# Optimization experiments

Measured on AMD Instinct MI355X. Metric: run time of the kernel, lower is better.

## Reference

```python
import jax, jax.numpy as jnp
import numpy as np


def rotate_half(x):
    d = x.shape[-1] // 2
    return jnp.concatenate([-x[..., d:], x[..., :d]], axis=-1)


def setup_inputs() -> dict:
    key = jax.random.key(0)
    ks = jax.random.split(key, 8)
    B, T, C, H = 2, 2048, 2048, 16
    hd = C // H
    x = jax.random.normal(ks[0], (B, T, C), dtype=jnp.float32)
    # realistic RoPE tables
    inv_freq = 1.0 / (10000.0 ** (jnp.arange(0, hd, 2, dtype=jnp.float32) / hd))
    t = jnp.arange(T, dtype=jnp.float32)
    freqs = jnp.einsum('t,f->tf', t, inv_freq)
    emb = jnp.concatenate([freqs, freqs], axis=-1)  # [T, hd]
    cos = jnp.cos(emb)
    sin = jnp.sin(emb)
    mask = jnp.tril(jnp.ones((T, T), dtype=bool))[None, None]  # causal [1,1,T,T]
    s = C ** -0.5
    Wq = jax.random.normal(ks[1], (C, C), dtype=jnp.float32) * s
    Wk = jax.random.normal(ks[2], (C, C), dtype=jnp.float32) * s
    Wv = jax.random.normal(ks[3], (C, C), dtype=jnp.float32) * s
    Wo = jax.random.normal(ks[4], (C, C), dtype=jnp.float32) * s
    return {"x": x, "cos": cos, "sin": sin, "mask": mask,
            "Wq": Wq, "Wk": Wk, "Wv": Wv, "Wo": Wo}


def reference(x, cos, sin, mask, Wq, Wk, Wv, Wo):
    B, T, C = x.shape
    H = 16
    hd = C // H
    scale = hd ** -0.5
    # projections: torch Linear stores W as [out,in], y = x @ W^T
    def proj(W):
        return jnp.einsum('btc,dc->btd', x, W).reshape(B, T, H, hd).transpose(0, 2, 1, 3)
    q, k, v = proj(Wq), proj(Wk), proj(Wv)  # [B,H,T,hd]
    c = cos[None, None]  # [1,1,T,hd]
    s = sin[None, None]
    q = q * c + rotate_half(q) * s
    k = k * c + rotate_half(k) * s
    attn = jnp.einsum('bhqd,bhkd->bhqk', q, k) * scale
    attn = jnp.where(mask, attn, -jnp.inf)
    attn = jax.nn.softmax(attn, axis=-1)
    out = jnp.einsum('bhqk,bhkd->bhqd', attn, v)
    out = out.transpose(0, 2, 1, 3).reshape(B, T, C)
    return jnp.einsum('btc,dc->btd', out, Wo)
```

## Files before the change

### kernel.cpp

```cpp
#include <hip/hip_runtime.h>
#include <cstdint>

typedef __bf16 bf16_t;
typedef __bf16 bf16x8 __attribute__((ext_vector_type(8)));
typedef __bf16 bf16x4 __attribute__((ext_vector_type(4)));
typedef float  f32x4  __attribute__((ext_vector_type(4)));

#define BB 2
#define TT 2048
#define CC 2048
#define HH 16
#define HD 128

static __device__ __forceinline__ void async_copy16(const void* gp, void* lp) {
  __builtin_amdgcn_global_load_lds(
      (const __attribute__((address_space(1))) void*)(uintptr_t)gp,
      (__attribute__((address_space(3))) void*)(uint32_t)(uintptr_t)lp,
      16, 0, 0);
}

__global__ __launch_bounds__(256)
void cast_all(const float* __restrict__ x, const float* __restrict__ wq,
              const float* __restrict__ wk, const float* __restrict__ wv,
              const float* __restrict__ wo, bf16_t* __restrict__ xb,
              bf16_t* __restrict__ wq_b) {
  const int NX4 = (BB * TT * CC) / 4;
  const int NW4 = (CC * CC) / 4;
  int i = blockIdx.x * 256 + threadIdx.x;
  const float* s;
  bf16_t* d;
  int off;
  if (i < NX4) {
    s = x; d = xb; off = i;
  } else {
    int j = i - NX4;
    int w = j >> 20;
    off = j & (NW4 - 1);
    s = (w == 0) ? wq : (w == 1) ? wk : (w == 2) ? wv : wo;
    d = wq_b + (size_t)w * (CC * CC);
  }
  float4 v = ((const float4*)s)[off];
  bf16x4 o;
  o[0] = (bf16_t)v.x; o[1] = (bf16_t)v.y; o[2] = (bf16_t)v.z; o[3] = (bf16_t)v.w;
  ((bf16x4*)d)[off] = o;
}

template <int MODE>
__global__ __launch_bounds__(256)
void gemm_bt(const bf16_t* __restrict__ A, const bf16_t* __restrict__ Bw,
             void* __restrict__ C0, void* __restrict__ C1, void* __restrict__ C2,
             int Kdim, int Ndim) {
  __shared__ __align__(16) char smem[128 * 136 * 2];
  bf16_t* As = (bf16_t*)smem;
  bf16_t* Bs = (bf16_t*)(smem + 16384);
  const int tid  = threadIdx.x;
  const int wave = tid >> 6, lane = tid & 63;
  const int quad = lane >> 4, l16 = lane & 15;
  const int m0 = blockIdx.y * 128, n0 = blockIdx.x * 128;
  const int wm = (wave >> 1) * 64, wn = (wave & 1) * 64;

  f32x4 acc[4][4] = {};

  const int srow = lane >> 3;
  const int scol = (((lane & 7) ^ srow) & 7) * 8;
  const int swz  = (l16 & 7) * 8;

  for (int k0 = 0; k0 < Kdim; k0 += 64) {
#pragma unroll
    for (int i = 0; i < 4; ++i) {
      int chunk = wave * 4 + i;
      int row = chunk * 8 + srow;
      async_copy16(A + (size_t)(m0 + row) * Kdim + k0 + scol, As + chunk * 512);
    }
#pragma unroll
    for (int i = 0; i < 4; ++i) {
      int chunk = wave * 4 + i;
      int row = chunk * 8 + srow;
      async_copy16(Bw + (size_t)(n0 + row) * Kdim + k0 + scol, Bs + chunk * 512);
    }
    __syncthreads();
#pragma unroll
    for (int kk = 0; kk < 64; kk += 32) {
      const int koff = (kk + quad * 8) ^ swz;
      bf16x8 af[4], bfr[4];
#pragma unroll
      for (int i = 0; i < 4; ++i)
        af[i] = *(const bf16x8*)&As[(wm + i * 16 + l16) * 64 + koff];
#pragma unroll
      for (int j = 0; j < 4; ++j)
        bfr[j] = *(const bf16x8*)&Bs[(wn + j * 16 + l16) * 64 + koff];
#pragma unroll
      for (int i = 0; i < 4; ++i)
#pragma unroll
        for (int j = 0; j < 4; ++j)
          acc[i][j] = __builtin_amdgcn_mfma_f32_16x16x32_bf16(af[i], bfr[j], acc[i][j], 0, 0, 0);
    }
    __syncthreads();
  }

#pragma unroll
  for (int i = 0; i < 4; ++i)
#pragma unroll
    for (int j = 0; j < 4; ++j) {
      int gcol = n0 + wn + j * 16 + l16;
#pragma unroll
      for (int r = 0; r < 4; ++r) {
        int grow = m0 + wm + i * 16 + quad * 4 + r;
        ((float*)C0)[(size_t)grow * Ndim + gcol] = acc[i][j][r];
      }
    }
}

__global__ __launch_bounds__(512, 2)
void gemm_qkv256(const bf16_t* __restrict__ A, const bf16_t* __restrict__ Bw,
                 bf16_t* __restrict__ Qo, bf16_t* __restrict__ Ko,
                 bf16_t* __restrict__ Vo, int Kdim) {
  extern __shared__ __align__(16) char smem[];
  bf16_t* lds = (bf16_t*)smem;
  const int tid  = threadIdx.x;
  const int wave = tid >> 6, lane = tid & 63;
  const int quad = lane >> 4, l16 = lane & 15;
  const int wm = wave >> 2, wn = wave & 3;
  const int n0 = blockIdx.x * 256, m0 = blockIdx.y * 256;

  const int srow = lane >> 3;
  const int scol = ((lane & 7) ^ srow) * 8;
  const int swz  = (l16 & 7) * 8;
  const int nK = Kdim >> 6;

  const bf16_t* Ag = A  + (size_t)(m0 + wave * 32 + srow) * Kdim + scol;
  const bf16_t* Bg = Bw + (size_t)(n0 + wave * 32 + srow) * Kdim + scol;
  const int ldsChunk = wave * 4 * 512;

#define STAGE_A(kt, buf)                                                      \
  {                                                                           \
    bf16_t* dstA = lds + (buf) * 32768 + ldsChunk;                            \
    const bf16_t* srcA = Ag + (kt) * 64;                                      \
    _Pragma("unroll")                                                         \
    for (int ci = 0; ci < 4; ++ci)                                            \
      async_copy16(srcA + (size_t)(ci * 8) * Kdim, dstA + ci * 512);          \
  }
#define STAGE_B(kt, buf)                                                      \
  {                                                                           \
    bf16_t* dstB = lds + (buf) * 32768 + 16384 + ldsChunk;                    \
    const bf16_t* srcB = Bg + (kt) * 64;                                      \
    _Pragma("unroll")                                                         \
    for (int ci = 0; ci < 4; ++ci)                                            \
      async_copy16(srcB + (size_t)(ci * 8) * Kdim, dstB + ci * 512);          \
  }

  f32x4 acc[8][4] = {};

  STAGE_A(0, 0); STAGE_B(0, 0); STAGE_A(1, 1); STAGE_B(1, 1);

  const int k0off = (quad * 8) ^ swz;
  const int k1off = (32 + quad * 8) ^ swz;

  for (int k = 0; k < nK; ++k) {
    const int cur = k & 1;
    const bf16_t* Asb = lds + cur * 32768;
    const bf16_t* Bsb = Asb + 16384;
    if (k < nK - 1) asm volatile("s_waitcnt vmcnt(8)" ::: "memory");
    else            asm volatile("s_waitcnt vmcnt(0)" ::: "memory");
    __builtin_amdgcn_s_barrier();
    __builtin_amdgcn_sched_barrier(0);

    bf16x8 a0[8], b0[4], a1[8], b1[4];
#pragma unroll
    for (int i = 0; i < 8; ++i)
      a0[i] = *(const bf16x8*)&Asb[(wm * 128 + i * 16 + l16) * 64 + k0off];
#pragma unroll
    for (int j = 0; j < 4; ++j)
      b0[j] = *(const bf16x8*)&Bsb[(wn * 64 + j * 16 + l16) * 64 + k0off];
    asm volatile("s_waitcnt lgkmcnt(0)" ::: "memory");
    __builtin_amdgcn_sched_barrier(0);
    __builtin_amdgcn_s_setprio(1);
#pragma unroll
    for (int i = 0; i < 4; ++i)
#pragma unroll
      for (int j = 0; j < 4; ++j)
        acc[i][j] = __builtin_amdgcn_mfma_f32_16x16x32_bf16(a0[i], b0[j], acc[i][j], 0, 0, 0);
    __builtin_amdgcn_s_setprio(0);

#pragma unroll
    for (int i = 0; i < 8; ++i)
      a1[i] = *(const bf16x8*)&Asb[(wm * 128 + i * 16 + l16) * 64 + k1off];
#pragma unroll
    for (int j = 0; j < 4; ++j)
      b1[j] = *(const bf16x8*)&Bsb[(wn * 64 + j * 16 + l16) * 64 + k1off];
    __builtin_amdgcn_s_setprio(1);
#pragma unroll
    for (int i = 4; i < 8; ++i)
#pragma unroll
      for (int j = 0; j < 4; ++j)
        acc[i][j] = __builtin_amdgcn_mfma_f32_16x16x32_bf16(a0[i], b0[j], acc[i][j], 0, 0, 0);
    __builtin_amdgcn_s_setprio(0);
    asm volatile("s_waitcnt lgkmcnt(0)" ::: "memory");
    __builtin_amdgcn_s_barrier();
    __builtin_amdgcn_sched_barrier(0);

    if (k + 2 < nK) STAGE_A(k + 2, cur);
    __builtin_amdgcn_s_setprio(1);
#pragma unroll
    for (int i = 0; i < 4; ++i)
#pragma unroll
      for (int j = 0; j < 4; ++j)
        acc[i][j] = __builtin_amdgcn_mfma_f32_16x16x32_bf16(a1[i], b1[j], acc[i][j], 0, 0, 0);
    __builtin_amdgcn_s_setprio(0);

    if (k + 2 < nK) STAGE_B(k + 2, cur);
    __builtin_amdgcn_s_setprio(1);
#pragma unroll
    for (int i = 4; i < 8; ++i)
#pragma unroll
      for (int j = 0; j < 4; ++j)
        acc[i][j] = __builtin_amdgcn_mfma_f32_16x16x32_bf16(a1[i], b1[j], acc[i][j], 0, 0, 0);
    __builtin_amdgcn_s_setprio(0);
  }
#undef STAGE_A
#undef STAGE_B

  const int proj = n0 >> 11;
  if (proj < 2) {
    bf16_t* dst = proj == 0 ? Qo : Ko;
#pragma unroll
    for (int i = 0; i < 8; ++i)
#pragma unroll
      for (int j = 0; j < 4; ++j) {
        int colv = (n0 & (CC - 1)) + wn * 64 + j * 16 + l16;
        int h = colv >> 7, d = colv & (HD - 1);
#pragma unroll
        for (int r = 0; r < 4; ++r) {
          int grow = m0 + wm * 128 + i * 16 + quad * 4 + r;
          int b = grow >> 11, t = grow & (TT - 1);
          dst[(((size_t)(b * HH + h) * TT + t) * HD) + d] = (bf16_t)acc[i][j][r];
        }
      }
  } else {
    bf16_t* Ct = (bf16_t*)smem;
    const int b = m0 >> 11;
#pragma unroll
    for (int p = 0; p < 2; ++p) {
      __syncthreads();
      if (wm == p) {
#pragma unroll
        for (int i = 0; i < 8; ++i)
#pragma unroll
          for (int j = 0; j < 4; ++j) {
            int c = wn * 64 + j * 16 + l16;
#pragma unroll
            for (int r = 0; r < 4; ++r)
              Ct[(i * 16 + quad * 4 + r) * 264 + c] = (bf16_t)acc[i][j][r];
          }
      }
      __syncthreads();
      const unsigned short* Cu = (const unsigned short*)Ct;
      int c  = tid & 255;
      int rh = (tid >> 8) * 64;
      int dv = (n0 & (CC - 1)) + c;
      int h = dv >> 7, d = dv & (HD - 1);
      unsigned int pk[32];
#pragma unroll
      for (int s = 0; s < 32; ++s) {
        unsigned int lo = Cu[(rh + 2 * s) * 264 + c];
        unsigned int hi = Cu[(rh + 2 * s + 1) * 264 + c];
        pk[s] = lo | (hi << 16);
      }
      bf16_t* dstp = Vo + ((size_t)(b * HH + h) * HD + d) * TT +
                     (m0 & (TT - 1)) + p * 128 + rh;
#pragma unroll
      for (int u = 0; u < 8; ++u) {
        uint4 w; w.x = pk[4*u]; w.y = pk[4*u+1]; w.z = pk[4*u+2]; w.w = pk[4*u+3];
        *(uint4*)(dstp + 8 * u) = w;
      }
    }
  }
}

__global__ __launch_bounds__(256) void rope_kernel(bf16_t* __restrict__ Q, bf16_t* __restrict__ K,
                                                   const float* __restrict__ cosT,
                                                   const float* __restrict__ sinT) {
  int idx = blockIdx.x * 256 + threadIdx.x;
  int d  = idx & 63;
  int t  = (idx >> 6) & (TT - 1);
  int bh = idx >> 17;
  size_t base = ((size_t)bh * TT + t) * HD;
  float c0 = cosT[t * HD + d],      s0 = sinT[t * HD + d];
  float c1 = cosT[t * HD + 64 + d], s1 = sinT[t * HD + 64 + d];
  float q0 = Q[base + d], q1 = Q[base + 64 + d];
  Q[base + d]      = (bf16_t)(q0 * c0 - q1 * s0);
  Q[base + 64 + d] = (bf16_t)(q1 * c1 + q0 * s1);
  float k0 = K[base + d], k1 = K[base + 64 + d];
  K[base + d]      = (bf16_t)(k0 * c0 - k1 * s0);
  K[base + 64 + d] = (bf16_t)(k1 * c1 + k0 * s1);
}

__global__ __launch_bounds__(512, 2)
void attn_kernel(const bf16_t* __restrict__ Q, const bf16_t* __restrict__ K,
                 const bf16_t* __restrict__ Vt, bf16_t* __restrict__ Out) {
  __shared__ __align__(16) bf16_t Ks[2][64 * 128];
  __shared__ __align__(16) bf16_t Vs[2][128 * 64];
  __shared__ __align__(16) bf16_t Pl[8][16 * 72];
  const int lane = threadIdx.x & 63, wave = threadIdx.x >> 6;
  const int quad = lane >> 4, l16 = lane & 15;
  const int linear = blockIdx.x;
  const int hb = linear & 31;
  const int h = hb & (HH - 1), b = hb >> 4;
  const int spair = linear >> 5;
  const size_t qkbase = (size_t)(b * HH + h) * TT * HD;
  const bf16_t* Kh = K + qkbase;
  const bf16_t* Vh = Vt + (size_t)(b * HH + h) * HD * TT;
  const float scale = 0.08838834764831845f;

  const int srK = lane >> 4;
  const int sgK = lane & 15;
  const int scK0 = (sgK ^ srK) * 8;
  const int scK1 = (sgK ^ (4 + srK)) * 8;
  const int srV = lane >> 3;
  const int scV = (((lane & 7) ^ srV) & 7) * 8;
  const int swz = (l16 & 7) * 8;

#pragma unroll
  for (int half = 0; half < 2; ++half) {
    const int qt = half == 0 ? (15 - spair) : spair;
    const int q0 = qt * 128 + wave * 16;
    const int nIter = qt * 2 + 2;

    bf16x8 qf[4];
    {
      const bf16_t* qrow = Q + qkbase + (size_t)(q0 + l16) * HD;
#pragma unroll
      for (int kc = 0; kc < 4; ++kc) qf[kc] = *(const bf16x8*)(qrow + kc * 32 + quad * 8);
    }

    f32x4 o[8] = {};
    float l_i[4] = {};

    {
#pragma unroll
      for (int i = 0; i < 2; ++i) {
        int chunk = wave * 2 + i;
        int sc = (chunk & 1) ? scK1 : scK0;
        async_copy16(Kh + (size_t)(chunk * 4 + srK) * HD + sc, &Ks[0][chunk * 512]);
      }
#pragma unroll
      for (int i = 0; i < 2; ++i) {
        int chunk = wave * 2 + i;
        async_copy16(Vh + (size_t)(chunk * 8 + srV) * TT + scV, &Vs[0][chunk * 512]);
      }
    }

    for (int it = 0; it < nIter; ++it) {
      const int cur = it & 1;
      const int key0 = it * 64;
      __syncthreads();

      if (it + 1 < nIter) {
        const int nxt = cur ^ 1;
        const int knxt = key0 + 64;
#pragma unroll
        for (int i = 0; i < 2; ++i) {
          int chunk = wave * 2 + i;
          int sc = (chunk & 1) ? scK1 : scK0;
          async_copy16(Kh + (size_t)(knxt + chunk * 4 + srK) * HD + sc, &Ks[nxt][chunk * 512]);
        }
#pragma unroll
        for (int i = 0; i < 2; ++i) {
          int chunk = wave * 2 + i;
          async_copy16(Vh + (size_t)(chunk * 8 + srV) * TT + knxt + scV, &Vs[nxt][chunk * 512]);
        }
      }

      f32x4 s[4] = {};
#pragma unroll
      for (int kc = 0; kc < 4; ++kc) {
        const int koff = (kc * 32 + quad * 8) ^ swz;
#pragma unroll
        for (int kt = 0; kt < 4; ++kt) {
          bf16x8 kf = *(const bf16x8*)&Ks[cur][(kt * 16 + l16) * 128 + koff];
          s[kt] = __builtin_amdgcn_mfma_f32_16x16x32_bf16(qf[kc], kf, s[kt], 0, 0, 0);
        }
      }

      {
        bf16_t* pl = &Pl[wave][0];
#pragma unroll
        for (int r = 0; r < 4; ++r) {
          int rel = q0 + quad * 4 + r - key0;
          int prow = (quad * 4 + r) * 72;
          float lr = 0.f;
#pragma unroll
          for (int kt = 0; kt < 4; ++kt) {
            int c16 = kt * 16 + l16;
            float e = (c16 > rel) ? 0.f : __expf(s[kt][r] * scale);
            lr += e;
            pl[prow + c16] = (bf16_t)e;
          }
          l_i[r] += lr;
        }
      }

      bf16x8 pf0 = *(const bf16x8*)&Pl[wave][l16 * 72 + quad * 8];
      bf16x8 pf1 = *(const bf16x8*)&Pl[wave][l16 * 72 + 32 + quad * 8];
      const int voff0 = (quad * 8) ^ swz;
      const int voff1 = (32 + quad * 8) ^ swz;
#pragma unroll
      for (int n = 0; n < 8; ++n) {
        bf16x8 vf0 = *(const bf16x8*)&Vs[cur][(n * 16 + l16) * 64 + voff0];
        bf16x8 vf1 = *(const bf16x8*)&Vs[cur][(n * 16 + l16) * 64 + voff1];
        o[n] = __builtin_amdgcn_mfma_f32_16x16x32_bf16(pf0, vf0, o[n], 0, 0, 0);
        o[n] = __builtin_amdgcn_mfma_f32_16x16x32_bf16(pf1, vf1, o[n], 0, 0, 0);
      }
    }

#pragma unroll
    for (int r = 0; r < 4; ++r) {
      float l = l_i[r];
#pragma unroll
      for (int off = 1; off < 16; off <<= 1) l += __shfl_xor(l, off);
      l_i[r] = 1.f / l;
    }

#pragma unroll
    for (int n = 0; n < 8; ++n)
#pragma unroll
      for (int r = 0; r < 4; ++r) {
        int qg = q0 + quad * 4 + r;
        size_t off = ((size_t)(b * TT + qg) * CC) + h * HD + n * 16 + l16;
        Out[off] = (bf16_t)(o[n][r] * l_i[r]);
      }
  }
}

extern "C" void kernel_launch(void* const* d_in, const int* in_sizes, int n_in,
                              void* d_out, int out_size, void* d_ws, size_t ws_size,
                              hipStream_t stream) {
  const float* x    = (const float*)d_in[0];
  const float* cosT = (const float*)d_in[1];
  const float* sinT = (const float*)d_in[2];
  const float* Wq = (const float*)d_in[4];
  const float* Wk = (const float*)d_in[5];
  const float* Wv = (const float*)d_in[6];
  const float* Wo = (const float*)d_in[7];
  float* out = (float*)d_out;

  char* ws = (char*)d_ws;
  const size_t XSZ = (size_t)BB * TT * CC * 2;
  const size_t WSZ = (size_t)CC * CC * 2;
  bf16_t* x_bf  = (bf16_t*)(ws);
  bf16_t* wq_bf = (bf16_t*)(ws + XSZ);
  bf16_t* wo_bf = (bf16_t*)(ws + XSZ + 3 * WSZ);
  bf16_t* Qb    = (bf16_t*)(ws + XSZ + 4 * WSZ);
  bf16_t* Kb    = (bf16_t*)(ws + 2 * XSZ + 4 * WSZ);
  bf16_t* Vt    = (bf16_t*)(ws + 3 * XSZ + 4 * WSZ);
  bf16_t* attn_bf = x_bf;

  const int NX = BB * TT * CC;
  const int NW = CC * CC;
  cast_all<<<(NX / 4 + 4 * (NW / 4)) / 256, 256, 0, stream>>>(
      x, Wq, Wk, Wv, Wo, x_bf, wq_bf);

  (void)hipFuncSetAttribute(reinterpret_cast<const void*>(gemm_qkv256),
                            hipFuncAttributeMaxDynamicSharedMemorySize, 131072);
  gemm_qkv256<<<dim3(3 * CC / 256, BB * TT / 256), 512, 131072, stream>>>(
      x_bf, wq_bf, Qb, Kb, Vt, CC);

  rope_kernel<<<(BB * HH * TT * 64) / 256, 256, 0, stream>>>(Qb, Kb, cosT, sinT);

  attn_kernel<<<dim3(BB * HH * 8), 512, 0, stream>>>(Qb, Kb, Vt, attn_bf);

  gemm_bt<0><<<dim3(CC / 128, BB * TT / 128), 256, 0, stream>>>(
      attn_bf, wo_bf, out, nullptr, nullptr, CC, CC);
}
```

Before: 375.0 us.

## Split V projection into separate 128-tile GEMM and vectorize RoPE kernel

The fused QKV GEMM now computes only Q and K, giving a 16x16 grid of 256-wide tiles. V is produced by the 128x128 gemm_bt kernel in a new mode that transposes through LDS into the Vt layout. This targets the partial final wave of the 24x16 fused grid, at the cost of an extra launch and a smaller-tile GEMM for V. The RoPE kernel now handles 8 elements per thread with 16-byte loads and stores instead of scalar accesses.

```diff
diff --git a/kernel.cpp b/kernel.cpp
--- a/kernel.cpp
+++ b/kernel.cpp
@@ -98,23 +98,56 @@
     __syncthreads();
   }
 
-#pragma unroll
-  for (int i = 0; i < 4; ++i)
-#pragma unroll
-    for (int j = 0; j < 4; ++j) {
-      int gcol = n0 + wn + j * 16 + l16;
-#pragma unroll
-      for (int r = 0; r < 4; ++r) {
-        int grow = m0 + wm + i * 16 + quad * 4 + r;
-        ((float*)C0)[(size_t)grow * Ndim + gcol] = acc[i][j][r];
-      }
-    }
+  if (MODE == 0) {
+#pragma unroll
+    for (int i = 0; i < 4; ++i)
+#pragma unroll
+      for (int j = 0; j < 4; ++j) {
+        int gcol = n0 + wn + j * 16 + l16;
+#pragma unroll
+        for (int r = 0; r < 4; ++r) {
+          int grow = m0 + wm + i * 16 + quad * 4 + r;
+          ((float*)C0)[(size_t)grow * Ndim + gcol] = acc[i][j][r];
+        }
+      }
+  } else {
+    const int h = (n0 & (CC - 1)) >> 7;
+    bf16_t* Ct = (bf16_t*)smem;
+    __syncthreads();
+#pragma unroll
+    for (int i = 0; i < 4; ++i)
+#pragma unroll
+      for (int j = 0; j < 4; ++j) {
+        int c = wn + j * 16 + l16;
+#pragma unroll
+        for (int r = 0; r < 4; ++r)
+          Ct[(wm + i * 16 + quad * 4 + r) * 136 + c] = (bf16_t)acc[i][j][r];
+      }
+    __syncthreads();
+    const unsigned short* Cu = (const unsigned short*)Ct;
+    int col = tid >> 1;
+    int rh  = (tid & 1) * 64;
+    int grow0 = m0 + rh;
+    int b = grow0 >> 11, t0 = grow0 & (TT - 1);
+    unsigned int pk[32];
+#pragma unroll
+    for (int s = 0; s < 32; ++s) {
+      unsigned int lo = Cu[(rh + 2 * s) * 136 + col];
+      unsigned int hi = Cu[(rh + 2 * s + 1) * 136 + col];
+      pk[s] = lo | (hi << 16);
+    }
+    bf16_t* dstp = (bf16_t*)C2 + ((size_t)(b * HH + h) * HD + col) * TT + t0;
+#pragma unroll
+    for (int u = 0; u < 8; ++u) {
+      uint4 w; w.x = pk[4*u]; w.y = pk[4*u+1]; w.z = pk[4*u+2]; w.w = pk[4*u+3];
+      *(uint4*)(dstp + 8 * u) = w;
+    }
+  }
 }
 
 __global__ __launch_bounds__(512, 2)
 void gemm_qkv256(const bf16_t* __restrict__ A, const bf16_t* __restrict__ Bw,
-                 bf16_t* __restrict__ Qo, bf16_t* __restrict__ Ko,
-                 bf16_t* __restrict__ Vo, int Kdim) {
+                 bf16_t* __restrict__ Qo, bf16_t* __restrict__ Ko, int Kdim) {
   extern __shared__ __align__(16) char smem[];
   bf16_t* lds = (bf16_t*)smem;
   const int tid  = threadIdx.x;
@@ -221,78 +254,63 @@
 #undef STAGE_B
 
   const int proj = n0 >> 11;
-  if (proj < 2) {
-    bf16_t* dst = proj == 0 ? Qo : Ko;
-#pragma unroll
-    for (int i = 0; i < 8; ++i)
-#pragma unroll
-      for (int j = 0; j < 4; ++j) {
-        int colv = (n0 & (CC - 1)) + wn * 64 + j * 16 + l16;
-        int h = colv >> 7, d = colv & (HD - 1);
-#pragma unroll
-        for (int r = 0; r < 4; ++r) {
-          int grow = m0 + wm * 128 + i * 16 + quad * 4 + r;
-          int b = grow >> 11, t = grow & (TT - 1);
-          dst[(((size_t)(b * HH + h) * TT + t) * HD) + d] = (bf16_t)acc[i][j][r];
-        }
-      }
-  } else {
-    bf16_t* Ct = (bf16_t*)smem;
-    const int b = m0 >> 11;
-#pragma unroll
-    for (int p = 0; p < 2; ++p) {
-      __syncthreads();
-      if (wm == p) {
-#pragma unroll
-        for (int i = 0; i < 8; ++i)
-#pragma unroll
-          for (int j = 0; j < 4; ++j) {
-            int c = wn * 64 + j * 16 + l16;
-#pragma unroll
-            for (int r = 0; r < 4; ++r)
-              Ct[(i * 16 + quad * 4 + r) * 264 + c] = (bf16_t)acc[i][j][r];
-          }
-      }
-      __syncthreads();
-      const unsigned short* Cu = (const unsigned short*)Ct;
-      int c  = tid & 255;
-      int rh = (tid >> 8) * 64;
-      int dv = (n0 & (CC - 1)) + c;
-      int h = dv >> 7, d = dv & (HD - 1);
-      unsigned int pk[32];
-#pragma unroll
-      for (int s = 0; s < 32; ++s) {
-        unsigned int lo = Cu[(rh + 2 * s) * 264 + c];
-        unsigned int hi = Cu[(rh + 2 * s + 1) * 264 + c];
-        pk[s] = lo | (hi << 16);
-      }
-      bf16_t* dstp = Vo + ((size_t)(b * HH + h) * HD + d) * TT +
-                     (m0 & (TT - 1)) + p * 128 + rh;
-#pragma unroll
-      for (int u = 0; u < 8; ++u) {
-        uint4 w; w.x = pk[4*u]; w.y = pk[4*u+1]; w.z = pk[4*u+2]; w.w = pk[4*u+3];
-        *(uint4*)(dstp + 8 * u) = w;
-      }
-    }
-  }
+  bf16_t* dst = proj == 0 ? Qo : Ko;
+#pragma unroll
+  for (int i = 0; i < 8; ++i)
+#pragma unroll
+    for (int j = 0; j < 4; ++j) {
+      int colv = (n0 & (CC - 1)) + wn * 64 + j * 16 + l16;
+      int h = colv >> 7, d = colv & (HD - 1);
+#pragma unroll
+      for (int r = 0; r < 4; ++r) {
+        int grow = m0 + wm * 128 + i * 16 + quad * 4 + r;
+        int b = grow >> 11, t = grow & (TT - 1);
+        dst[(((size_t)(b * HH + h) * TT + t) * HD) + d] = (bf16_t)acc[i][j][r];
+      }
+    }
 }
 
 __global__ __launch_bounds__(256) void rope_kernel(bf16_t* __restrict__ Q, bf16_t* __restrict__ K,
                                                    const float* __restrict__ cosT,
                                                    const float* __restrict__ sinT) {
   int idx = blockIdx.x * 256 + threadIdx.x;
-  int d  = idx & 63;
-  int t  = (idx >> 6) & (TT - 1);
-  int bh = idx >> 17;
+  int g  = idx & 7;
+  int t  = (idx >> 3) & (TT - 1);
+  int bh = idx >> 14;
+  int d0 = g * 8;
   size_t base = ((size_t)bh * TT + t) * HD;
-  float c0 = cosT[t * HD + d],      s0 = sinT[t * HD + d];
-  float c1 = cosT[t * HD + 64 + d], s1 = sinT[t * HD + 64 + d];
-  float q0 = Q[base + d], q1 = Q[base + 64 + d];
-  Q[base + d]      = (bf16_t)(q0 * c0 - q1 * s0);
-  Q[base + 64 + d] = (bf16_t)(q1 * c1 + q0 * s1);
-  float k0 = K[base + d], k1 = K[base + 64 + d];
-  K[base + d]      = (bf16_t)(k0 * c0 - k1 * s0);
-  K[base + 64 + d] = (bf16_t)(k1 * c1 + k0 * s1);
+
+  float4 cl0 = *(const float4*)(cosT + t * HD + d0);
+  float4 cl1 = *(const float4*)(cosT + t * HD + d0 + 4);
+  float4 sl0 = *(const float4*)(sinT + t * HD + d0);
+  float4 sl1 = *(const float4*)(sinT + t * HD + d0 + 4);
+  float4 ch0 = *(const float4*)(cosT + t * HD + 64 + d0);
+  float4 ch1 = *(const float4*)(cosT + t * HD + 64 + d0 + 4);
+  float4 sh0 = *(const float4*)(sinT + t * HD + 64 + d0);
+  float4 sh1 = *(const float4*)(sinT + t * HD + 64 + d0 + 4);
+  float cl[8] = {cl0.x, cl0.y, cl0.z, cl0.w, cl1.x, cl1.y, cl1.z, cl1.w};
+  float sl[8] = {sl0.x, sl0.y, sl0.z, sl0.w, sl1.x, sl1.y, sl1.z, sl1.w};
+  float ch[8] = {ch0.x, ch0.y, ch0.z, ch0.w, ch1.x, ch1.y, ch1.z, ch1.w};
+  float sh[8] = {sh0.x, sh0.y, sh0.z, sh0.w, sh1.x, sh1.y, sh1.z, sh1.w};
+
+  bf16x8 qlo = *(const bf16x8*)(Q + base + d0);
+  bf16x8 qhi = *(const bf16x8*)(Q + base + 64 + d0);
+  bf16x8 klo = *(const bf16x8*)(K + base + d0);
+  bf16x8 khi = *(const bf16x8*)(K + base + 64 + d0);
+  bf16x8 qlo2, qhi2, klo2, khi2;
+#pragma unroll
+  for (int e = 0; e < 8; ++e) {
+    float ql = (float)qlo[e], qh = (float)qhi[e];
+    qlo2[e] = (bf16_t)(ql * cl[e] - qh * sl[e]);
+    qhi2[e] = (bf16_t)(qh * ch[e] + ql * sh[e]);
+    float kl = (float)klo[e], kh = (float)khi[e];
+    klo2[e] = (bf16_t)(kl * cl[e] - kh * sl[e]);
+    khi2[e] = (bf16_t)(kh * ch[e] + kl * sh[e]);
+  }
+  *(bf16x8*)(Q + base + d0)      = qlo2;
+  *(bf16x8*)(Q + base + 64 + d0) = qhi2;
+  *(bf16x8*)(K + base + d0)      = klo2;
+  *(bf16x8*)(K + base + 64 + d0) = khi2;
 }
 
 __global__ __launch_bounds__(512, 2)
@@ -449,6 +467,7 @@
   const size_t WSZ = (size_t)CC * CC * 2;
   bf16_t* x_bf  = (bf16_t*)(ws);
   bf16_t* wq_bf = (bf16_t*)(ws + XSZ);
+  bf16_t* wv_bf = (bf16_t*)(ws + XSZ + 2 * WSZ);
   bf16_t* wo_bf = (bf16_t*)(ws + XSZ + 3 * WSZ);
   bf16_t* Qb    = (bf16_t*)(ws + XSZ + 4 * WSZ);
   bf16_t* Kb    = (bf16_t*)(ws + 2 * XSZ + 4 * WSZ);
@@ -462,10 +481,13 @@
 
   (void)hipFuncSetAttribute(reinterpret_cast<const void*>(gemm_qkv256),
                             hipFuncAttributeMaxDynamicSharedMemorySize, 131072);
-  gemm_qkv256<<<dim3(3 * CC / 256, BB * TT / 256), 512, 131072, stream>>>(
-      x_bf, wq_bf, Qb, Kb, Vt, CC);
-
-  rope_kernel<<<(BB * HH * TT * 64) / 256, 256, 0, stream>>>(Qb, Kb, cosT, sinT);
+  gemm_qkv256<<<dim3(2 * CC / 256, BB * TT / 256), 512, 131072, stream>>>(
+      x_bf, wq_bf, Qb, Kb, CC);
+
+  gemm_bt<1><<<dim3(CC / 128, BB * TT / 128), 256, 0, stream>>>(
+      x_bf, wv_bf, nullptr, nullptr, Vt, CC, CC);
+
+  rope_kernel<<<(BB * HH * TT * 8) / 256, 256, 0, stream>>>(Qb, Kb, cosT, sinT);
 
   attn_kernel<<<dim3(BB * HH * 8), 512, 0, stream>>>(Qb, Kb, Vt, attn_bf);
 
```

Measured after the change: 370.7 us. About the same (-1.1%).
